# Kernel tuning notes

Hardware: AMD Instinct MI355X
Metric: run time of the kernel (lower is better)

The kernel has to match this reference:

```python
import jax, jax.numpy as jnp
import numpy as np

B, N, L, D_IN, D = 32, 2048, 32768, 4, 64


def setup_inputs() -> dict:
    key = jax.random.key(0)
    ks = jax.random.split(key, 10)
    s = 0.05  # modest init scale for params
    return {
        "pred_node": jax.random.normal(ks[0], (B, N, D_IN), jnp.float32),
        "line_param": jax.random.normal(ks[1], (B, L, 4), jnp.float32),
        "W_embed": jax.random.normal(ks[2], (D_IN, D), jnp.float32) * s,
        "b_embed": jnp.zeros((D,), jnp.float32),
        "W1": jax.random.normal(ks[3], (2 * D, D), jnp.float32) * s,
        "b1": jnp.zeros((D,), jnp.float32),
        "W2": jax.random.normal(ks[4], (D, 4), jnp.float32) * s,
        "b2": jnp.zeros((4,), jnp.float32),
        "edge_src": jax.random.randint(ks[5], (B, L), 0, N, jnp.int32),
        "edge_dst": jax.random.randint(ks[6], (B, L), 0, N, jnp.int32),
    }


def reference(pred_node, line_param, W_embed, b_embed, W1, b1, W2, b2,
              edge_src, edge_dst):
    # node_feat_to_line_feat: Linear(4 -> d_model) over all nodes at once
    node_feat = jnp.einsum("bni,id->bnd", pred_node, W_embed) + b_embed  # (B,N,D)

    # Batched gather of node-feature pairs per edge (replaces Python loops)
    fi = jnp.take_along_axis(node_feat, edge_src[..., None].astype(jnp.int32), axis=1)  # (B,L,D)
    fj = jnp.take_along_axis(node_feat, edge_dst[..., None].astype(jnp.int32), axis=1)  # (B,L,D)
    combined = jnp.concatenate([fi, fj], axis=-1)  # (B,L,2D)

    # line_pred_head: Linear(2D->D) -> ReLU -> Dropout(eval: identity) -> Linear(D->4)
    h = jax.nn.relu(jnp.einsum("ble,ed->bld", combined, W1) + b1)
    line_pred = jnp.einsum("bld,do->blo", h, W2) + b2  # (B,L,4)

    # Cols 0,1 copied from line_param; cols 2,3 from the prediction head
    out = jnp.concatenate([line_param[..., :2], line_pred[..., 2:4]], axis=-1)
    return out
```

## Files before the change

### kernel.cpp

```cpp
#include <hip/hip_runtime.h>
#include <hip/hip_fp16.h>
#include <stdint.h>

#define B_ 32
#define N_ 2048
#define L_ 32768


static __device__ __forceinline__ __half2 pkrn(float a, float b) {
    return __float22half2_rn(make_float2(a, b));
}

static __device__ __forceinline__ __half2 pkmax(__half2 a, __half2 b) {
    __half2 r;
    asm("v_pk_max_f16 %0, %1, %2" : "=v"(r) : "v"(a), "v"(b));
    return r;
}

static __device__ __forceinline__ __half2 bits_h2(float x) {
    union { float f; __half2 h; } u;
    u.f = x;
    return u.h;
}

__global__ __launch_bounds__(512) void prep_kernel(
    const float* __restrict__ W_embed, const float* __restrict__ b_embed,
    const float* __restrict__ W1, const float* __restrict__ b1,
    const float* __restrict__ W2, __half2* __restrict__ wh) {
    __shared__ float sacc[64][8];
    __shared__ float sbias[64];
    int tid = threadIdx.x;
    int d = tid & 63;
    int i = (tid >> 6) & 3;
    int half_ = tid >> 8;

    const float* w1base = W1 + (half_ ? 64 * 64 : 0);
    float acc = 0.f;
#pragma unroll
    for (int k = 0; k < 64; ++k) {
        acc = fmaf(W_embed[i * 64 + k], w1base[k * 64 + d], acc);
    }
    sacc[d][half_ * 4 + i] = acc;

    if (tid < 64) {
        float bb = 0.f;
#pragma unroll
        for (int k = 0; k < 64; ++k) {
            bb = fmaf(b_embed[k], W1[k * 64 + d] + W1[(64 + k) * 64 + d], bb);
        }
        sbias[d] = bb + b1[d];
    }
    __syncthreads();

    if (tid < 64) {
#pragma unroll
        for (int k = 0; k < 8; ++k) {
            float v = sacc[tid][k];
            wh[tid * 12 + k] = pkrn(v, v);
        }
        float bv = sbias[tid];
        wh[tid * 12 + 8] = pkrn(bv, bv);
        float c2 = W2[tid * 4 + 2];
        float c3 = W2[tid * 4 + 3];
        wh[tid * 12 + 9] = pkrn(c2, c2);
        wh[tid * 12 + 10] = pkrn(c3, c3);
        wh[tid * 12 + 11] = pkrn(0.f, 0.f);
    }
}

__global__ __launch_bounds__(256, 8) void edge_kernel(
    const float4* __restrict__ pred_node,
    const __half2* __restrict__ wh,
    const int* __restrict__ esrc, const int* __restrict__ edst,
    const float4* __restrict__ lp4,
    const float* __restrict__ b2,
    float4* __restrict__ out) {
    const int tid = threadIdx.x;
    const int bid = blockIdx.x;
    const int x = bid & 7;
    const int i = bid >> 3;
    const int b = x + 8 * (i >> 5);
    const int j = i & 31;
    const int ebase = b * L_ + j * 1024 + tid;

    int sa[4], ta[4];
#pragma unroll
    for (int p = 0; p < 4; ++p) {
        sa[p] = esrc[ebase + p * 256];
        ta[p] = edst[ebase + p * 256];
    }

    const float4* pnb = pred_node + b * N_;
    __half2 px[2][8];
#pragma unroll
    for (int pr = 0; pr < 2; ++pr) {
        float4 s0 = pnb[sa[2 * pr]];
        float4 s1 = pnb[sa[2 * pr + 1]];
        float4 t0 = pnb[ta[2 * pr]];
        float4 t1 = pnb[ta[2 * pr + 1]];
        px[pr][0] = pkrn(s0.x, s1.x);
        px[pr][1] = pkrn(s0.y, s1.y);
        px[pr][2] = pkrn(s0.z, s1.z);
        px[pr][3] = pkrn(s0.w, s1.w);
        px[pr][4] = pkrn(t0.x, t1.x);
        px[pr][5] = pkrn(t0.y, t1.y);
        px[pr][6] = pkrn(t0.z, t1.z);
        px[pr][7] = pkrn(t0.w, t1.w);
    }

    const __half2 zero = pkrn(0.f, 0.f);
    __half2 acc2[2] = {zero, zero};
    __half2 acc3[2] = {zero, zero};

#pragma unroll
    for (int f = 0; f < 64; ++f) {
        const float4* wv = reinterpret_cast<const float4*>(wh) + f * 3;
        float4 q0 = wv[0], q1 = wv[1], q2 = wv[2];
        __half2 w0 = bits_h2(q0.x), w1 = bits_h2(q0.y);
        __half2 w2w = bits_h2(q0.z), w3w = bits_h2(q0.w);
        __half2 w4 = bits_h2(q1.x), w5 = bits_h2(q1.y);
        __half2 w6w = bits_h2(q1.z), w7w = bits_h2(q1.w);
        __half2 bs = bits_h2(q2.x);
        __half2 c2 = bits_h2(q2.y), c3 = bits_h2(q2.z);
#pragma unroll
        for (int pr = 0; pr < 2; ++pr) {
            __half2 h = bs;
            h = __hfma2(px[pr][0], w0, h);
            h = __hfma2(px[pr][1], w1, h);
            h = __hfma2(px[pr][2], w2w, h);
            h = __hfma2(px[pr][3], w3w, h);
            h = __hfma2(px[pr][4], w4, h);
            h = __hfma2(px[pr][5], w5, h);
            h = __hfma2(px[pr][6], w6w, h);
            h = __hfma2(px[pr][7], w7w, h);
            h = pkmax(h, zero);
            acc2[pr] = __hfma2(h, c2, acc2[pr]);
            acc3[pr] = __hfma2(h, c3, acc3[pr]);
        }
    }

    float bias2 = b2[2], bias3 = b2[3];
#pragma unroll
    for (int p = 0; p < 4; ++p) {
        int e = ebase + p * 256;
        float4 lp = lp4[e];
        int pr = p >> 1;
        float r2 = (p & 1) ? __high2float(acc2[pr]) : __low2float(acc2[pr]);
        float r3 = (p & 1) ? __high2float(acc3[pr]) : __low2float(acc3[pr]);
        out[e] = make_float4(lp.x, lp.y, bias2 + r2, bias3 + r3);
    }
}

extern "C" void kernel_launch(void* const* d_in, const int* in_sizes, int n_in,
                              void* d_out, int out_size, void* d_ws, size_t ws_size,
                              hipStream_t stream) {
    const float* pred_node = (const float*)d_in[0];
    const float* line_param = (const float*)d_in[1];
    const float* W_embed = (const float*)d_in[2];
    const float* b_embed = (const float*)d_in[3];
    const float* W1 = (const float*)d_in[4];
    const float* b1 = (const float*)d_in[5];
    const float* W2 = (const float*)d_in[6];
    const float* b2 = (const float*)d_in[7];
    const int* esrc = (const int*)d_in[8];
    const int* edst = (const int*)d_in[9];
    float* out = (float*)d_out;

    __half2* wh = (__half2*)d_ws;

    prep_kernel<<<1, 512, 0, stream>>>(W_embed, b_embed, W1, b1, W2, wh);
    edge_kernel<<<1024, 256, 0, stream>>>((const float4*)pred_node, wh,
                                          esrc, edst,
                                          (const float4*)line_param, b2,
                                          (float4*)out);
}
```

Before: 109.4 us.

## Stage per-batch node table in shared memory as fp16 and halve edges per thread

Each block now loads the whole batch's node table (2048 float4) into LDS as packed fp16 and serves the src/dst gathers from there instead of from scattered global reads. Edges per thread drop from 4 to 2, and the grid doubles to 2048 blocks to keep the device occupied. The line_param loads are issued early so they overlap with staging. The price is that every block reloads 32KB of node data (each batch is reloaded by 64 blocks), adds a block-wide barrier, and uses 16KB of LDS per block, which may limit occupancy.

New measurement: 106.3 us. -2.8%, faster.

```diff
diff --git a/kernel.cpp b/kernel.cpp
--- a/kernel.cpp
+++ b/kernel.cpp
@@ -17,10 +17,19 @@
     return r;
 }
 
-static __device__ __forceinline__ __half2 bits_h2(float x) {
-    union { float f; __half2 h; } u;
-    u.f = x;
-    return u.h;
+static __device__ __forceinline__ unsigned int h2u(__half2 h) {
+    union { __half2 h; unsigned int u; } c; c.h = h; return c.u;
+}
+
+static __device__ __forceinline__ __half2 u2h(unsigned int u) {
+    union { unsigned int u; __half2 h; } c; c.u = u; return c.h;
+}
+
+static __device__ __forceinline__ __half2 lo_lo(unsigned int A, unsigned int B) {
+    return u2h(__builtin_amdgcn_perm(A, B, 0x01000504u));
+}
+static __device__ __forceinline__ __half2 hi_hi(unsigned int A, unsigned int B) {
+    return u2h(__builtin_amdgcn_perm(A, B, 0x03020706u));
 }
 
 __global__ __launch_bounds__(512) void prep_kernel(
@@ -75,80 +84,73 @@
     const float4* __restrict__ lp4,
     const float* __restrict__ b2,
     float4* __restrict__ out) {
+    __shared__ uint2 spn[N_];
+
     const int tid = threadIdx.x;
     const int bid = blockIdx.x;
     const int x = bid & 7;
     const int i = bid >> 3;
-    const int b = x + 8 * (i >> 5);
-    const int j = i & 31;
-    const int ebase = b * L_ + j * 1024 + tid;
+    const int b = x + 8 * (i >> 6);
+    const int j = i & 63;
+    const int ebase = b * L_ + j * 512 + tid;
 
-    int sa[4], ta[4];
+    int s0 = esrc[ebase], s1 = esrc[ebase + 256];
+    int t0 = edst[ebase], t1 = edst[ebase + 256];
+    float4 lpa = lp4[ebase];
+    float4 lpb = lp4[ebase + 256];
+
+    const float4* pnb = pred_node + b * N_;
 #pragma unroll
-    for (int p = 0; p < 4; ++p) {
-        sa[p] = esrc[ebase + p * 256];
-        ta[p] = edst[ebase + p * 256];
+    for (int q = 0; q < 8; ++q) {
+        int idx = tid + q * 256;
+        float4 v = pnb[idx];
+        spn[idx] = make_uint2(h2u(pkrn(v.x, v.y)), h2u(pkrn(v.z, v.w)));
     }
 
-    const float4* pnb = pred_node + b * N_;
-    __half2 px[2][8];
-#pragma unroll
-    for (int pr = 0; pr < 2; ++pr) {
-        float4 s0 = pnb[sa[2 * pr]];
-        float4 s1 = pnb[sa[2 * pr + 1]];
-        float4 t0 = pnb[ta[2 * pr]];
-        float4 t1 = pnb[ta[2 * pr + 1]];
-        px[pr][0] = pkrn(s0.x, s1.x);
-        px[pr][1] = pkrn(s0.y, s1.y);
-        px[pr][2] = pkrn(s0.z, s1.z);
-        px[pr][3] = pkrn(s0.w, s1.w);
-        px[pr][4] = pkrn(t0.x, t1.x);
-        px[pr][5] = pkrn(t0.y, t1.y);
-        px[pr][6] = pkrn(t0.z, t1.z);
-        px[pr][7] = pkrn(t0.w, t1.w);
-    }
+    __syncthreads();
 
-    const __half2 zero = pkrn(0.f, 0.f);
-    __half2 acc2[2] = {zero, zero};
-    __half2 acc3[2] = {zero, zero};
+    uint2 a0 = spn[s0];
+    uint2 a1 = spn[s1];
+    uint2 d0 = spn[t0];
+    uint2 d1 = spn[t1];
 
-#pragma unroll
+    __half2 px0 = lo_lo(a0.x, a1.x);
+    __half2 px1 = hi_hi(a0.x, a1.x);
+    __half2 px2 = lo_lo(a0.y, a1.y);
+    __half2 px3 = hi_hi(a0.y, a1.y);
+    __half2 px4 = lo_lo(d0.x, d1.x);
+    __half2 px5 = hi_hi(d0.x, d1.x);
+    __half2 px6 = lo_lo(d0.y, d1.y);
+    __half2 px7 = hi_hi(d0.y, d1.y);
+
+    const __half2 zero = u2h(0u);
+    __half2 acc2 = zero, acc3 = zero;
+
+#pragma unroll 4
     for (int f = 0; f < 64; ++f) {
         const float4* wv = reinterpret_cast<const float4*>(wh) + f * 3;
         float4 q0 = wv[0], q1 = wv[1], q2 = wv[2];
-        __half2 w0 = bits_h2(q0.x), w1 = bits_h2(q0.y);
-        __half2 w2w = bits_h2(q0.z), w3w = bits_h2(q0.w);
-        __half2 w4 = bits_h2(q1.x), w5 = bits_h2(q1.y);
-        __half2 w6w = bits_h2(q1.z), w7w = bits_h2(q1.w);
-        __half2 bs = bits_h2(q2.x);
-        __half2 c2 = bits_h2(q2.y), c3 = bits_h2(q2.z);
-#pragma unroll
-        for (int pr = 0; pr < 2; ++pr) {
-            __half2 h = bs;
-            h = __hfma2(px[pr][0], w0, h);
-            h = __hfma2(px[pr][1], w1, h);
-            h = __hfma2(px[pr][2], w2w, h);
-            h = __hfma2(px[pr][3], w3w, h);
-            h = __hfma2(px[pr][4], w4, h);
-            h = __hfma2(px[pr][5], w5, h);
-            h = __hfma2(px[pr][6], w6w, h);
-            h = __hfma2(px[pr][7], w7w, h);
-            h = pkmax(h, zero);
-            acc2[pr] = __hfma2(h, c2, acc2[pr]);
-            acc3[pr] = __hfma2(h, c3, acc3[pr]);
-        }
+        __half2 h = u2h(__float_as_uint(q2.x));
+        h = __hfma2(px0, u2h(__float_as_uint(q0.x)), h);
+        h = __hfma2(px1, u2h(__float_as_uint(q0.y)), h);
+        h = __hfma2(px2, u2h(__float_as_uint(q0.z)), h);
+        h = __hfma2(px3, u2h(__float_as_uint(q0.w)), h);
+        h = __hfma2(px4, u2h(__float_as_uint(q1.x)), h);
+        h = __hfma2(px5, u2h(__float_as_uint(q1.y)), h);
+        h = __hfma2(px6, u2h(__float_as_uint(q1.z)), h);
+        h = __hfma2(px7, u2h(__float_as_uint(q1.w)), h);
+        h = pkmax(h, zero);
+        acc2 = __hfma2(h, u2h(__float_as_uint(q2.y)), acc2);
+        acc3 = __hfma2(h, u2h(__float_as_uint(q2.z)), acc3);
     }
 
     float bias2 = b2[2], bias3 = b2[3];
-#pragma unroll
-    for (int p = 0; p < 4; ++p) {
-        int e = ebase + p * 256;
-        float4 lp = lp4[e];
-        int pr = p >> 1;
-        float r2 = (p & 1) ? __high2float(acc2[pr]) : __low2float(acc2[pr]);
-        float r3 = (p & 1) ? __high2float(acc3[pr]) : __low2float(acc3[pr]);
-        out[e] = make_float4(lp.x, lp.y, bias2 + r2, bias3 + r3);
-    }
+    out[ebase] = make_float4(lpa.x, lpa.y,
+                             bias2 + __low2float(acc2),
+                             bias3 + __low2float(acc3));
+    out[ebase + 256] = make_float4(lpb.x, lpb.y,
+                                   bias2 + __high2float(acc2),
+                                   bias3 + __high2float(acc3));
 }
 
 extern "C" void kernel_launch(void* const* d_in, const int* in_sizes, int n_in,
@@ -169,7 +171,7 @@
     __half2* wh = (__half2*)d_ws;
 
     prep_kernel<<<1, 512, 0, stream>>>(W_embed, b_embed, W1, b1, W2, wh);
-    edge_kernel<<<1024, 256, 0, stream>>>((const float4*)pred_node, wh,
+    edge_kernel<<<2048, 256, 0, stream>>>((const float4*)pred_node, wh,
                                           esrc, edst,
                                           (const float4*)line_param, b2,
                                           (float4*)out);
```
